# Kernel optimization log

Hardware: AMD Instinct MI355X
Metric: run time of the kernel (lower is better)

Reference implementation:

```python
import jax, jax.numpy as jnp
import numpy as np

B, C, N, K, COUT = 2, 192, 16384, 16, 192
EPS = 1e-5


def setup_inputs() -> dict:
    key = jax.random.key(0)
    k1, k2, k3 = jax.random.split(key, 3)
    x = jax.random.normal(k1, (B, C, N, 1), dtype=jnp.float32)
    edge_index = jax.random.randint(k2, (2, B, N, K), 0, N, dtype=jnp.int32)
    # kaiming-normal-ish 1x1 conv weight, flattened to [C_out, 2C]
    W = jax.random.normal(k3, (COUT, 2 * C), dtype=jnp.float32) * np.float32(np.sqrt(2.0 / (2 * C)))
    b_conv = jnp.zeros((COUT,), jnp.float32)
    gamma = jnp.ones((COUT,), jnp.float32)
    beta = jnp.zeros((COUT,), jnp.float32)
    return {"x": x, "W": W, "b_conv": b_conv, "gamma": gamma, "beta": beta, "edge_index": edge_index}


def reference(x, W, b_conv, gamma, beta, edge_index):
    b, c, n, _ = x.shape
    k = edge_index.shape[-1]
    xs = x[..., 0]  # [B,C,N]

    def gather(idx):  # idx: [B,N,K] -> [B,C,N,K]
        return jnp.take_along_axis(xs, idx.reshape(b, 1, n * k), axis=2).reshape(b, c, n, k)

    x_i = gather(edge_index[1])
    x_j = gather(edge_index[0])
    mr = jnp.max(x_j - x_i, axis=-1)  # max-relative feature [B,C,N]

    # torch.cat([x.unsqueeze(2), x_j.unsqueeze(2)], 2).reshape(b, 2c, n, 1) interleaves channels
    cat = jnp.stack([xs, mr], axis=2).reshape(b, 2 * c, n)  # [B,2C,N]

    # 1x1 conv == channel matmul
    h = jnp.einsum('oc,bcn->bon', W, cat) + b_conv[None, :, None]  # [B,COUT,N]

    # BatchNorm2d (training-mode batch statistics over batch+spatial dims)
    mean = h.mean(axis=(0, 2), keepdims=True)
    var = h.var(axis=(0, 2), keepdims=True)
    h = (h - mean) / jnp.sqrt(var + EPS) * gamma[None, :, None] + beta[None, :, None]

    out = jax.nn.gelu(h, approximate=False)
    return out[..., None]  # [B,COUT,N,1]
```

## Files before the change

### kernel.cpp

```cpp
#include <hip/hip_runtime.h>
#include <math.h>

#define BB 2
#define CC 192
#define NN 16384
#define KK 16
#define COUT 192
#define MM (BB * NN)
#define KDIM (2 * CC)
#define EPSF 1e-5f
#define NGB 256

typedef __attribute__((ext_vector_type(8))) short short8;
typedef __attribute__((ext_vector_type(4))) float f32x4;

static __device__ __forceinline__ float bf16_to_f32(unsigned int u16) {
    return __uint_as_float(u16 << 16);
}
static __device__ __forceinline__ float bf16hi_to_f32(unsigned int u) {
    return __uint_as_float(u & 0xffff0000u);
}
static __device__ __forceinline__ unsigned short f32_to_bf16(float f) {
    unsigned int u = __float_as_uint(f);
    unsigned int r = (u + 0x7fffu + ((u >> 16) & 1u)) >> 16;
    return (unsigned short)r;
}

#define TRB (512 * 3 * BB)
__global__ __launch_bounds__(256) void k_prep(const float* __restrict__ x,
                                              unsigned int* __restrict__ xt32,
                                              const float* __restrict__ W,
                                              unsigned short* __restrict__ Wb) {
    int bid = blockIdx.x;
    int t = threadIdx.x;
    if (bid >= TRB) {
        int wb = bid - TRB;
        int base = wb * 1024 + t * 4;
        float4 v = *(const float4*)(W + base);
        uint2 o;
        o.x = (unsigned int)f32_to_bf16(v.x) | ((unsigned int)f32_to_bf16(v.y) << 16);
        o.y = (unsigned int)f32_to_bf16(v.z) | ((unsigned int)f32_to_bf16(v.w) << 16);
        *(uint2*)(Wb + base) = o;
        return;
    }
    __shared__ float tile[64][33];
    int nb = bid & 511;
    int rest = bid >> 9;
    int cb = rest % 3;
    int b = rest / 3;
    int n0 = nb * 32, c0 = cb * 64;
    int tx = t & 31, ty = t >> 5;
    #pragma unroll
    for (int j = 0; j < 64; j += 8)
        tile[ty + j][tx] = x[((size_t)b * CC + (c0 + ty + j)) * NN + n0 + tx];
    __syncthreads();
    #pragma unroll
    for (int j = 0; j < 32; j += 8) {
        int n = n0 + ty + j;
        unsigned int w = (unsigned int)f32_to_bf16(tile[2 * tx][ty + j]) |
                         ((unsigned int)f32_to_bf16(tile[2 * tx + 1][ty + j]) << 16);
        xt32[(((size_t)b * NN + n) * CC + c0) / 2 + tx] = w;
    }
}

__global__ __launch_bounds__(384) void k_gather(const unsigned short* __restrict__ xt,
                                                const int* __restrict__ edge,
                                                uint4* __restrict__ xcat4) {
    __shared__ int sj[8][KK], si[8][KK];
    int t = threadIdx.x;
    int m0 = blockIdx.x * 8;
    int b = m0 >> 14, n0 = m0 & (NN - 1);
    if (t < 128)
        ((int*)sj)[t] = edge[((size_t)b * NN + n0) * KK + t];
    else if (t < 256)
        ((int*)si)[t - 128] = edge[((size_t)(BB + b) * NN + n0) * KK + (t - 128)];
    __syncthreads();

    int p = t / 48, c2 = t % 48;
    const uint2* base = (const uint2*)(xt + (size_t)b * NN * CC) + c2;
    float mx0 = -INFINITY, mx1 = -INFINITY, mx2 = -INFINITY, mx3 = -INFINITY;
    #pragma unroll
    for (int k = 0; k < KK; ++k) {
        uint2 uj = base[(size_t)sj[p][k] * 48];
        uint2 ui = base[(size_t)si[p][k] * 48];
        mx0 = fmaxf(mx0, bf16_to_f32(uj.x & 0xffffu) - bf16_to_f32(ui.x & 0xffffu));
        mx1 = fmaxf(mx1, bf16hi_to_f32(uj.x) - bf16hi_to_f32(ui.x));
        mx2 = fmaxf(mx2, bf16_to_f32(uj.y & 0xffffu) - bf16_to_f32(ui.y & 0xffffu));
        mx3 = fmaxf(mx3, bf16hi_to_f32(uj.y) - bf16hi_to_f32(ui.y));
    }
    uint2 xs = base[(size_t)(n0 + p) * 48];
    uint4 o;
    o.x = (xs.x & 0xffffu) | ((unsigned int)f32_to_bf16(mx0) << 16);
    o.y = (xs.x >> 16) | ((unsigned int)f32_to_bf16(mx1) << 16);
    o.z = (xs.y & 0xffffu) | ((unsigned int)f32_to_bf16(mx2) << 16);
    o.w = (xs.y >> 16) | ((unsigned int)f32_to_bf16(mx3) << 16);
    xcat4[(size_t)(m0 + p) * 48 + c2] = o;
}

#define BMT 128
__global__ __launch_bounds__(512) void k_gemm(const unsigned short* __restrict__ xcat,
                                              const unsigned short* __restrict__ Wb,
                                              unsigned short* __restrict__ h,
                                              float* __restrict__ psum,
                                              float* __restrict__ psum2) {
    __shared__ __align__(16) char ldsA[BMT * 128];
    __shared__ __align__(16) char ldsB[COUT * 128];
    int t = threadIdx.x;
    int m0 = blockIdx.x * BMT;
    int w = t >> 6, l = t & 63, lo = l & 15, q4 = l >> 4;
    f32x4 acc[12];
    #pragma unroll
    for (int i = 0; i < 12; ++i) acc[i] = (f32x4){0.f, 0.f, 0.f, 0.f};
    int rA = w * 16 + lo;

    for (int ks = 0; ks < KDIM / 64; ++ks) {
        int k0 = ks * 64;
        if (ks) __syncthreads();
        #pragma unroll
        for (int it = 0; it < 2; ++it) {
            int idx = t + it * 512;
            int r = idx >> 3, c = idx & 7;
            uint4 v = *(const uint4*)(xcat + (size_t)(m0 + r) * KDIM + k0 + c * 8);
            *(uint4*)(ldsA + r * 128 + ((c * 16) ^ ((r & 7) << 4))) = v;
        }
        #pragma unroll
        for (int it = 0; it < 3; ++it) {
            int idx = t + it * 512;
            int r = idx >> 3, c = idx & 7;
            uint4 v = *(const uint4*)(Wb + (size_t)r * KDIM + k0 + c * 8);
            *(uint4*)(ldsB + r * 128 + ((c * 16) ^ ((r & 7) << 4))) = v;
        }
        __syncthreads();
        #pragma unroll
        for (int kh = 0; kh < 2; ++kh) {
            int cb = kh * 64 + q4 * 16;
            short8 a = *(const short8*)(ldsA + rA * 128 + (cb ^ ((rA & 7) << 4)));
            #pragma unroll
            for (int ot = 0; ot < 12; ++ot) {
                int rB = ot * 16 + lo;
                short8 bf = *(const short8*)(ldsB + rB * 128 + (cb ^ ((rB & 7) << 4)));
                acc[ot] = __builtin_amdgcn_mfma_f32_16x16x32_bf16(a, bf, acc[ot], 0, 0, 0);
            }
        }
    }
    __syncthreads();

    float* reds = (float*)ldsA;
    float* reds2 = reds + 8 * COUT;
    int mrow = m0 + w * 16 + q4 * 4;
    #pragma unroll
    for (int ot = 0; ot < 12; ++ot) {
        int o = ot * 16 + lo;
        float s = 0.f, s2 = 0.f;
        #pragma unroll
        for (int r = 0; r < 4; ++r) {
            float v = acc[ot][r];
            h[(size_t)(mrow + r) * COUT + o] = f32_to_bf16(v);
            s += v;
            s2 += v * v;
        }
        s += __shfl_xor(s, 16);  s2 += __shfl_xor(s2, 16);
        s += __shfl_xor(s, 32);  s2 += __shfl_xor(s2, 32);
        if (q4 == 0) {
            reds[w * COUT + o] = s;
            reds2[w * COUT + o] = s2;
        }
    }
    __syncthreads();
    if (t < COUT) {
        float a = 0.f, a2 = 0.f;
        #pragma unroll
        for (int w8 = 0; w8 < 8; ++w8) {
            a += reds[w8 * COUT + t];
            a2 += reds2[w8 * COUT + t];
        }
        psum[blockIdx.x * COUT + t] = a;
        psum2[blockIdx.x * COUT + t] = a2;
    }
}

__global__ __launch_bounds__(384) void k_bn(const float* __restrict__ psum,
                                            const float* __restrict__ psum2,
                                            const float* __restrict__ gamma,
                                            const float* __restrict__ beta,
                                            float* __restrict__ sc_sh) {
    __shared__ float sa[COUT], sa2[COUT];
    int t = threadIdx.x;
    int o = t & (COUT - 1);
    if (t < COUT) {
        float a = 0.f;
        #pragma unroll 8
        for (int i = 0; i < NGB; ++i) a += psum[i * COUT + t];
        sa[t] = a;
    } else {
        int oo = t - COUT;
        float a2 = 0.f;
        #pragma unroll 8
        for (int i = 0; i < NGB; ++i) a2 += psum2[i * COUT + oo];
        sa2[oo] = a2;
    }
    __syncthreads();
    if (t < COUT) {
        float inv_m = 1.0f / (float)MM;
        float mean = sa[t] * inv_m;
        float var = sa2[t] * inv_m - mean * mean;
        float sc = gamma[t] * rsqrtf(var + EPSF);
        sc_sh[t] = sc;
        sc_sh[COUT + t] = beta[t] - mean * sc;
    }
    (void)o;
}

__global__ __launch_bounds__(256) void k_out(const unsigned short* __restrict__ h,
                                             const float* __restrict__ sc_sh,
                                             float* __restrict__ out) {
    __shared__ float tile[32][33];
    int b = blockIdx.z;
    int n0 = blockIdx.x * 32;
    int o0 = blockIdx.y * 32;
    int tx = threadIdx.x, ty = threadIdx.y;
    int o = o0 + tx;
    float sc = sc_sh[o];
    float sh = sc_sh[COUT + o];
    #pragma unroll
    for (int j = 0; j < 32; j += 8) {
        float v = bf16_to_f32(h[((size_t)b * NN + n0 + ty + j) * COUT + o]);
        v = v * sc + sh;
        tile[ty + j][tx] = 0.5f * v * (1.0f + erff(v * 0.70710678118654752440f));
    }
    __syncthreads();
    #pragma unroll
    for (int j = 0; j < 32; j += 8)
        out[((size_t)b * COUT + (o0 + ty + j)) * NN + n0 + tx] = tile[tx][ty + j];
}

extern "C" void kernel_launch(void* const* d_in, const int* in_sizes, int n_in,
                              void* d_out, int out_size, void* d_ws, size_t ws_size,
                              hipStream_t stream) {
    const float* x = (const float*)d_in[0];
    const float* W = (const float*)d_in[1];
    const float* gamma = (const float*)d_in[3];
    const float* beta = (const float*)d_in[4];
    const int* edge = (const int*)d_in[5];
    float* out = (float*)d_out;

    char* ws = (char*)d_ws;
    unsigned short* xt = (unsigned short*)ws;
    ws += (size_t)MM * CC * 2;
    unsigned short* xcat = (unsigned short*)ws;
    ws += (size_t)MM * KDIM * 2;
    unsigned short* Wb = (unsigned short*)ws;
    ws += (size_t)COUT * KDIM * 2;
    unsigned short* h = (unsigned short*)ws;
    ws += (size_t)MM * COUT * 2;
    float* psum = (float*)ws;
    ws += (size_t)NGB * COUT * sizeof(float);
    float* psum2 = (float*)ws;
    ws += (size_t)NGB * COUT * sizeof(float);
    float* sc_sh = (float*)ws;

    k_prep<<<TRB + 72, 256, 0, stream>>>(x, (unsigned int*)xt, W, Wb);

    k_gather<<<MM / 8, 384, 0, stream>>>(xt, edge, (uint4*)xcat);

    k_gemm<<<MM / BMT, 512, 0, stream>>>(xcat, Wb, h, psum, psum2);

    k_bn<<<1, 384, 0, stream>>>(psum, psum2, gamma, beta, sc_sh);

    dim3 ogrid(NN / 32, COUT / 32, BB);
    k_out<<<ogrid, dim3(32, 8), 0, stream>>>(h, sc_sh, out);
}
```

Before: 80.62 us.

## Widen gather loads, use direct global-to-LDS loads in GEMM, parallelize BN reduction

```diff
diff --git a/kernel.cpp b/kernel.cpp
--- a/kernel.cpp
+++ b/kernel.cpp
@@ -14,6 +14,9 @@
 typedef __attribute__((ext_vector_type(8))) short short8;
 typedef __attribute__((ext_vector_type(4))) float f32x4;
 
+#define AS1P const __attribute__((address_space(1))) void*
+#define AS3P __attribute__((address_space(3))) void*
+
 static __device__ __forceinline__ float bf16_to_f32(unsigned int u16) {
     return __uint_as_float(u16 << 16);
 }
@@ -66,35 +69,46 @@
 __global__ __launch_bounds__(384) void k_gather(const unsigned short* __restrict__ xt,
                                                 const int* __restrict__ edge,
                                                 uint4* __restrict__ xcat4) {
-    __shared__ int sj[8][KK], si[8][KK];
-    int t = threadIdx.x;
-    int m0 = blockIdx.x * 8;
+    __shared__ int sj[16][KK], si[16][KK];
+    int t = threadIdx.x;
+    int m0 = blockIdx.x * 16;
     int b = m0 >> 14, n0 = m0 & (NN - 1);
-    if (t < 128)
+    if (t < 256)
         ((int*)sj)[t] = edge[((size_t)b * NN + n0) * KK + t];
-    else if (t < 256)
+    if (t >= 128)
         ((int*)si)[t - 128] = edge[((size_t)(BB + b) * NN + n0) * KK + (t - 128)];
     __syncthreads();
 
-    int p = t / 48, c2 = t % 48;
-    const uint2* base = (const uint2*)(xt + (size_t)b * NN * CC) + c2;
-    float mx0 = -INFINITY, mx1 = -INFINITY, mx2 = -INFINITY, mx3 = -INFINITY;
+    int p = t / 24, c4 = t % 24;
+    const uint4* base = (const uint4*)(xt + (size_t)b * NN * CC) + c4;
+    float mx[8];
+    #pragma unroll
+    for (int c = 0; c < 8; ++c) mx[c] = -INFINITY;
     #pragma unroll
     for (int k = 0; k < KK; ++k) {
-        uint2 uj = base[(size_t)sj[p][k] * 48];
-        uint2 ui = base[(size_t)si[p][k] * 48];
-        mx0 = fmaxf(mx0, bf16_to_f32(uj.x & 0xffffu) - bf16_to_f32(ui.x & 0xffffu));
-        mx1 = fmaxf(mx1, bf16hi_to_f32(uj.x) - bf16hi_to_f32(ui.x));
-        mx2 = fmaxf(mx2, bf16_to_f32(uj.y & 0xffffu) - bf16_to_f32(ui.y & 0xffffu));
-        mx3 = fmaxf(mx3, bf16hi_to_f32(uj.y) - bf16hi_to_f32(ui.y));
-    }
-    uint2 xs = base[(size_t)(n0 + p) * 48];
-    uint4 o;
-    o.x = (xs.x & 0xffffu) | ((unsigned int)f32_to_bf16(mx0) << 16);
-    o.y = (xs.x >> 16) | ((unsigned int)f32_to_bf16(mx1) << 16);
-    o.z = (xs.y & 0xffffu) | ((unsigned int)f32_to_bf16(mx2) << 16);
-    o.w = (xs.y >> 16) | ((unsigned int)f32_to_bf16(mx3) << 16);
-    xcat4[(size_t)(m0 + p) * 48 + c2] = o;
+        uint4 vj = base[(size_t)sj[p][k] * 24];
+        uint4 vi = base[(size_t)si[p][k] * 24];
+        const unsigned int dj[4] = {vj.x, vj.y, vj.z, vj.w};
+        const unsigned int di[4] = {vi.x, vi.y, vi.z, vi.w};
+        #pragma unroll
+        for (int d = 0; d < 4; ++d) {
+            mx[2 * d]     = fmaxf(mx[2 * d],     bf16_to_f32(dj[d] & 0xffffu) - bf16_to_f32(di[d] & 0xffffu));
+            mx[2 * d + 1] = fmaxf(mx[2 * d + 1], bf16hi_to_f32(dj[d]) - bf16hi_to_f32(di[d]));
+        }
+    }
+    uint4 xs = base[(size_t)(n0 + p) * 24];
+    uint4 o0, o1;
+    o0.x = (xs.x & 0xffffu) | ((unsigned int)f32_to_bf16(mx[0]) << 16);
+    o0.y = (xs.x >> 16)     | ((unsigned int)f32_to_bf16(mx[1]) << 16);
+    o0.z = (xs.y & 0xffffu) | ((unsigned int)f32_to_bf16(mx[2]) << 16);
+    o0.w = (xs.y >> 16)     | ((unsigned int)f32_to_bf16(mx[3]) << 16);
+    o1.x = (xs.z & 0xffffu) | ((unsigned int)f32_to_bf16(mx[4]) << 16);
+    o1.y = (xs.z >> 16)     | ((unsigned int)f32_to_bf16(mx[5]) << 16);
+    o1.z = (xs.w & 0xffffu) | ((unsigned int)f32_to_bf16(mx[6]) << 16);
+    o1.w = (xs.w >> 16)     | ((unsigned int)f32_to_bf16(mx[7]) << 16);
+    size_t orow = (size_t)(m0 + p) * 48;
+    xcat4[orow + 2 * c4] = o0;
+    xcat4[orow + 2 * c4 + 1] = o1;
 }
 
 #define BMT 128
@@ -108,6 +122,7 @@
     int t = threadIdx.x;
     int m0 = blockIdx.x * BMT;
     int w = t >> 6, l = t & 63, lo = l & 15, q4 = l >> 4;
+    int lr = l >> 3, lc = l & 7;
     f32x4 acc[12];
     #pragma unroll
     for (int i = 0; i < 12; ++i) acc[i] = (f32x4){0.f, 0.f, 0.f, 0.f};
@@ -117,18 +132,18 @@
         int k0 = ks * 64;
         if (ks) __syncthreads();
         #pragma unroll
-        for (int it = 0; it < 2; ++it) {
-            int idx = t + it * 512;
-            int r = idx >> 3, c = idx & 7;
-            uint4 v = *(const uint4*)(xcat + (size_t)(m0 + r) * KDIM + k0 + c * 8);
-            *(uint4*)(ldsA + r * 128 + ((c * 16) ^ ((r & 7) << 4))) = v;
-        }
-        #pragma unroll
-        for (int it = 0; it < 3; ++it) {
-            int idx = t + it * 512;
-            int r = idx >> 3, c = idx & 7;
-            uint4 v = *(const uint4*)(Wb + (size_t)r * KDIM + k0 + c * 8);
-            *(uint4*)(ldsB + r * 128 + ((c * 16) ^ ((r & 7) << 4))) = v;
+        for (int e = 0; e < 2; ++e) {
+            int r = w * 16 + e * 8 + lr;
+            int cg = lc ^ (r & 7);
+            const unsigned short* gp = xcat + (size_t)(m0 + r) * KDIM + k0 + cg * 8;
+            __builtin_amdgcn_global_load_lds((AS1P)gp, (AS3P)(ldsA + w * 2048 + e * 1024), 16, 0, 0);
+        }
+        #pragma unroll
+        for (int e = 0; e < 3; ++e) {
+            int r = w * 24 + e * 8 + lr;
+            int cg = lc ^ (r & 7);
+            const unsigned short* gp = Wb + (size_t)r * KDIM + k0 + cg * 8;
+            __builtin_amdgcn_global_load_lds((AS1P)gp, (AS3P)(ldsB + w * 3072 + e * 1024), 16, 0, 0);
         }
         __syncthreads();
         #pragma unroll
@@ -179,36 +194,35 @@
     }
 }
 
-__global__ __launch_bounds__(384) void k_bn(const float* __restrict__ psum,
+__global__ __launch_bounds__(256) void k_bn(const float* __restrict__ psum,
                                             const float* __restrict__ psum2,
                                             const float* __restrict__ gamma,
                                             const float* __restrict__ beta,
                                             float* __restrict__ sc_sh) {
-    __shared__ float sa[COUT], sa2[COUT];
-    int t = threadIdx.x;
-    int o = t & (COUT - 1);
-    if (t < COUT) {
-        float a = 0.f;
-        #pragma unroll 8
-        for (int i = 0; i < NGB; ++i) a += psum[i * COUT + t];
-        sa[t] = a;
-    } else {
-        int oo = t - COUT;
-        float a2 = 0.f;
-        #pragma unroll 8
-        for (int i = 0; i < NGB; ++i) a2 += psum2[i * COUT + oo];
-        sa2[oo] = a2;
-    }
-    __syncthreads();
-    if (t < COUT) {
+    __shared__ float red[2][32][8];
+    int t = threadIdx.x;
+    int ch = t & 7, rr = t >> 3;
+    int o = blockIdx.x * 8 + ch;
+    float a = 0.f, a2 = 0.f;
+    for (int r = rr; r < NGB; r += 32) {
+        a += psum[r * COUT + o];
+        a2 += psum2[r * COUT + o];
+    }
+    red[0][rr][ch] = a;
+    red[1][rr][ch] = a2;
+    __syncthreads();
+    if (t < 8) {
+        float s = 0.f, s2 = 0.f;
+        #pragma unroll
+        for (int i = 0; i < 32; ++i) { s += red[0][i][t]; s2 += red[1][i][t]; }
+        int oo = blockIdx.x * 8 + t;
         float inv_m = 1.0f / (float)MM;
-        float mean = sa[t] * inv_m;
-        float var = sa2[t] * inv_m - mean * mean;
-        float sc = gamma[t] * rsqrtf(var + EPSF);
-        sc_sh[t] = sc;
-        sc_sh[COUT + t] = beta[t] - mean * sc;
-    }
-    (void)o;
+        float mean = s * inv_m;
+        float var = s2 * inv_m - mean * mean;
+        float sc = gamma[oo] * rsqrtf(var + EPSF);
+        sc_sh[oo] = sc;
+        sc_sh[COUT + oo] = beta[oo] - mean * sc;
+    }
 }
 
 __global__ __launch_bounds__(256) void k_out(const unsigned short* __restrict__ h,
@@ -261,11 +275,11 @@
 
     k_prep<<<TRB + 72, 256, 0, stream>>>(x, (unsigned int*)xt, W, Wb);
 
-    k_gather<<<MM / 8, 384, 0, stream>>>(xt, edge, (uint4*)xcat);
+    k_gather<<<MM / 16, 384, 0, stream>>>(xt, edge, (uint4*)xcat);
 
     k_gemm<<<MM / BMT, 512, 0, stream>>>(xcat, Wb, h, psum, psum2);
 
-    k_bn<<<1, 384, 0, stream>>>(psum, psum2, gamma, beta, sc_sh);
+    k_bn<<<24, 256, 0, stream>>>(psum, psum2, gamma, beta, sc_sh);
 
     dim3 ogrid(NN / 32, COUT / 32, BB);
     k_out<<<ogrid, dim3(32, 8), 0, stream>>>(h, sc_sh, out);
```

After: 73.66 us. 1.09x faster.
